# Kernel tuning notes

Measured on AMD Instinct MI355X. Metric: run time of the kernel, lower is better.

## Reference

```python
import jax, jax.numpy as jnp
import numpy as np

B_, J_, D_, E_, N_, K_ = 32, 1024, 192, 384, 16, 3


def _dwconv(x, w, b):
    # x: (B,J,E), w: (E,1,K) depthwise, b: (E,)
    xc = jnp.transpose(x, (0, 2, 1))  # (B,E,J)
    pad = w.shape[2] // 2
    y = jax.lax.conv_general_dilated(
        xc, w, window_strides=(1,), padding=[(pad, pad)],
        feature_group_count=w.shape[0], dimension_numbers=('NCH', 'OIH', 'NCH'))
    return jnp.transpose(y + b[None, :, None], (0, 2, 1))  # (B,J,E)


def _scan_dir(x, cw, cb, WB, bB, WC, bC, WD, bD, A, Wi, bi, Wr, br):
    # One directional selective-SSM pass. x: (B,J,E); A: (N,) negative diag.
    xc = _dwconv(x, cw, cb)                       # (B,J,E)
    Bt = xc @ WB + bB                             # (B,J,N)
    Ct = xc @ WC + bC                             # (B,J,N)
    Dt = jax.nn.softplus(xc @ WD + bD)            # Delta, (B,J,N)
    A_bar = jnp.exp(Dt * A)                       # ZOH discretization
    B_bar = (A_bar - 1.0) / (A + 1e-6) * Bt
    u = xc @ Wi + bi                              # in_to_state, (B,J,N)
    Bu = B_bar * u

    def step(h, ab_bu):
        ab, bu = ab_bu
        h = ab * h + bu
        return h, h

    h0 = jnp.zeros((x.shape[0], A.shape[0]), x.dtype)
    _, hs = jax.lax.scan(step, h0, (jnp.swapaxes(A_bar, 0, 1), jnp.swapaxes(Bu, 0, 1)))
    hs = jnp.swapaxes(hs, 0, 1)                   # (B,J,N)
    return (hs * Ct) @ Wr + br                    # readout, (B,J,E)


def setup_inputs() -> dict:
    key = jax.random.key(0)
    ks = iter(jax.random.split(key, 40))

    def nrm(shape, scale=0.02):
        return jax.random.normal(next(ks), shape, jnp.float32) * scale

    inp = {
        'tokens': jax.random.normal(next(ks), (B_, J_, D_), jnp.float32),
        'norm_g': jnp.ones((D_,), jnp.float32),
        'norm_b': jnp.zeros((D_,), jnp.float32),
        'Wx': nrm((D_, E_)), 'bx': jnp.zeros((E_,), jnp.float32),
        'Wz': nrm((D_, E_)), 'bz': jnp.zeros((E_,), jnp.float32),
        'convf_w': nrm((E_, 1, K_), 0.1), 'convf_b': jnp.zeros((E_,), jnp.float32),
        'convb_w': nrm((E_, 1, K_), 0.1), 'convb_b': jnp.zeros((E_,), jnp.float32),
        'WBf': nrm((E_, N_)), 'bBf': jnp.zeros((N_,), jnp.float32),
        'WCf': nrm((E_, N_)), 'bCf': jnp.zeros((N_,), jnp.float32),
        'WDf': nrm((E_, N_)), 'bDf': jnp.zeros((N_,), jnp.float32),
        'WBb': nrm((E_, N_)), 'bBb': jnp.zeros((N_,), jnp.float32),
        'WCb': nrm((E_, N_)), 'bCb': jnp.zeros((N_,), jnp.float32),
        'WDb': nrm((E_, N_)), 'bDb': jnp.zeros((N_,), jnp.float32),
        'A_log': nrm((N_,), 0.5),
        'Wi': nrm((E_, N_)), 'bi': jnp.zeros((N_,), jnp.float32),
        'Wr': nrm((N_, E_)), 'br': jnp.zeros((E_,), jnp.float32),
        'Wo': nrm((E_, D_)), 'bo': jnp.zeros((D_,), jnp.float32),
    }
    return inp


def reference(tokens, norm_g, norm_b, Wx, bx, Wz, bz, convf_w, convf_b,
              convb_w, convb_b, WBf, bBf, WCf, bCf, WDf, bDf, WBb, bBb,
              WCb, bCb, WDb, bDb, A_log, Wi, bi, Wr, br, Wo, bo):
    # LayerNorm (biased variance, eps=1e-5, like torch)
    mu = jnp.mean(tokens, axis=-1, keepdims=True)
    var = jnp.mean(jnp.square(tokens - mu), axis=-1, keepdims=True)
    t = (tokens - mu) / jnp.sqrt(var + 1e-5) * norm_g + norm_b

    x = t @ Wx + bx
    z = t @ Wz + bz
    gate = jax.nn.sigmoid(jax.nn.silu(z))

    # A computed under no_grad in torch -> stop_gradient here
    A = jax.lax.stop_gradient(-jax.nn.softplus(A_log))

    y_f = _scan_dir(x, convf_w, convf_b, WBf, bBf, WCf, bCf, WDf, bDf, A, Wi, bi, Wr, br)
    y_b = jnp.flip(_scan_dir(jnp.flip(x, 1), convb_w, convb_b, WBb, bBb, WCb, bCb,
                             WDb, bDb, A, Wi, bi, Wr, br), 1)
    y = (y_f + y_b) * gate
    return tokens + y @ Wo + bo
```

## Files before the change

kernel.cpp:

```cpp
#include <hip/hip_runtime.h>
#include <math.h>


typedef __attribute__((ext_vector_type(8))) short short8;
typedef __attribute__((ext_vector_type(4))) float f32x4;

__device__ __forceinline__ unsigned short f2bf(float f){
  union { float f; unsigned u; } v; v.f = f;
  unsigned r = v.u + 0x7FFFu + ((v.u >> 16) & 1u);
  return (unsigned short)(r >> 16);
}
__device__ __forceinline__ float bf2f(unsigned short s){
  union { unsigned u; float f; } v; v.u = ((unsigned)s) << 16;
  return v.f;
}
__device__ __forceinline__ float softplusf(float x){
  return (x > 20.f) ? x : log1pf(expf(x));
}
__device__ __forceinline__ float sigf_fast(float x){
  return __builtin_amdgcn_rcpf(1.f + __expf(-x));
}

__global__ __launch_bounds__(256) void prep_kernel(
    const float* __restrict__ Wx, const float* __restrict__ Wz,
    const float* __restrict__ WBf, const float* __restrict__ WCf,
    const float* __restrict__ WDf, const float* __restrict__ WBb,
    const float* __restrict__ WCb, const float* __restrict__ WDb,
    const float* __restrict__ Wi, const float* __restrict__ Wr,
    const float* __restrict__ Wo,
    const float* __restrict__ bBf, const float* __restrict__ bCf,
    const float* __restrict__ bDf, const float* __restrict__ bBb,
    const float* __restrict__ bCb, const float* __restrict__ bDb,
    const float* __restrict__ bi,
    unsigned short* __restrict__ Wxz_t, unsigned short* __restrict__ W4f_t,
    unsigned short* __restrict__ W4b_t, unsigned short* __restrict__ Wrt2,
    unsigned short* __restrict__ Wot, float* __restrict__ b4f,
    float* __restrict__ b4b)
{
  int idx = blockIdx.x * 256 + threadIdx.x;
  if (idx < 147456){ int n = idx / 192, k = idx % 192;
    Wxz_t[idx] = f2bf(n < 384 ? Wx[k*384 + n] : Wz[k*384 + n - 384]); return; }
  idx -= 147456;
  if (idx < 24576){ int n = idx / 384, k = idx % 384;
    const float* W = (n<16)?WBf:(n<32)?WCf:(n<48)?WDf:Wi;
    W4f_t[idx] = f2bf(W[k*16 + (n&15)]); return; }
  idx -= 24576;
  if (idx < 24576){ int n = idx / 384, k = idx % 384;
    const float* W = (n<16)?WBb:(n<32)?WCb:(n<48)?WDb:Wi;
    W4b_t[idx] = f2bf(W[k*16 + (n&15)]); return; }
  idx -= 24576;
  if (idx < 12288){ int n = idx / 32, k = idx % 32;
    Wrt2[idx] = f2bf(Wr[(k&15)*384 + n]); return; }
  idx -= 12288;
  if (idx < 73728){ int n = idx / 384, k = idx % 384;
    Wot[idx] = f2bf(Wo[k*192 + n]); return; }
  idx -= 73728;
  if (idx < 64){
    const float* bsel = (idx<16)?bBf:(idx<32)?bCf:(idx<48)?bDf:bi;
    b4f[idx] = bsel[idx & 15]; return; }
  idx -= 64;
  if (idx < 64){
    const float* bsel = (idx<16)?bBb:(idx<32)?bCb:(idx<48)?bDb:bi;
    b4b[idx] = bsel[idx & 15]; return; }
}

__global__ __launch_bounds__(512) void ln_xz_mfma(
    const float* __restrict__ tokens, const float* __restrict__ g,
    const float* __restrict__ nb, const unsigned short* __restrict__ Wxz_t,
    const float* __restrict__ bx, const float* __restrict__ bz,
    unsigned short* __restrict__ x_bf, unsigned short* __restrict__ gate_bf)
{
  __shared__ unsigned short t_lds[32 * 200];
  __shared__ unsigned short out_lds[16 * 784];
  const int t = threadIdx.x;
  const int row0 = blockIdx.x * 32;

  {
    const int r = t >> 4, l16 = t & 15;
    const float* tr = tokens + (long)(row0 + r) * 192;
    float v[12], s = 0.f, sq = 0.f;
#pragma unroll
    for (int i = 0; i < 12; i++){ float x = tr[l16 + 16*i]; v[i] = x; s += x; sq += x*x; }
#pragma unroll
    for (int m = 1; m < 16; m <<= 1){ s += __shfl_xor(s, m); sq += __shfl_xor(sq, m); }
    const float mu = s * (1.f/192.f);
    const float rstd = rsqrtf(sq * (1.f/192.f) - mu*mu + 1e-5f);
#pragma unroll
    for (int i = 0; i < 12; i++){
      const int d = l16 + 16*i;
      t_lds[r*200 + d] = f2bf((v[i] - mu)*rstd*g[d] + nb[d]);
    }
  }
  __syncthreads();

  const int lane = t & 63, w = t >> 6;
  const int c0 = w * 96;
  const int l15 = lane & 15, q = lane >> 4;
  f32x4 acc[2][6];
#pragma unroll
  for (int m = 0; m < 2; m++)
#pragma unroll
    for (int n = 0; n < 6; n++) acc[m][n] = (f32x4){0.f,0.f,0.f,0.f};

  const unsigned short* wb = Wxz_t + (long)(c0 + l15)*192 + q*8;
#pragma unroll
  for (int ks = 0; ks < 6; ks++){
    const int k0 = ks * 32;
    short8 a0 = *(const short8*)&t_lds[l15*200 + k0 + q*8];
    short8 a1 = *(const short8*)&t_lds[(16 + l15)*200 + k0 + q*8];
#pragma unroll
    for (int nf = 0; nf < 6; nf++){
      short8 bw = *(const short8*)&wb[nf*16*192 + k0];
      acc[0][nf] = __builtin_amdgcn_mfma_f32_16x16x32_bf16(a0, bw, acc[0][nf], 0, 0, 0);
      acc[1][nf] = __builtin_amdgcn_mfma_f32_16x16x32_bf16(a1, bw, acc[1][nf], 0, 0, 0);
    }
  }

#pragma unroll
  for (int m = 0; m < 2; m++){
#pragma unroll
    for (int nf = 0; nf < 6; nf++){
      const int c = c0 + nf*16 + l15;
      const int scol = c0 + ((nf + q) % 6)*16 + l15;
      if (c < 384){
        const float bv = bx[c];
#pragma unroll
        for (int r = 0; r < 4; r++)
          out_lds[(q*4 + r)*784 + scol] = f2bf(acc[m][nf][r] + bv);
      } else {
        const float bv = bz[c - 384];
#pragma unroll
        for (int r = 0; r < 4; r++){
          const float z = acc[m][nf][r] + bv;
          const float si = z * sigf_fast(z);
          out_lds[(q*4 + r)*784 + scol] = f2bf(sigf_fast(si));
        }
      }
    }
    __syncthreads();
    {
#pragma unroll
      for (int i = 0; i < 3; i++){
        const int item = i*512 + t;
        const int row  = item / 96;
        const int c_out = (item % 96) * 8;
        const int qq = (row >> 2) & 3;
        const int wsl = c_out / 96;
        const int nfl = (c_out % 96) / 16;
        const int scol = wsl*96 + ((nfl + qq) % 6)*16 + (c_out % 16);
        short8 v = *(const short8*)&out_lds[row*784 + scol];
        const long R = (long)row0 + m*16 + row;
        if (c_out < 384) *(short8*)&x_bf[R*384 + c_out] = v;
        else             *(short8*)&gate_bf[R*384 + (c_out - 384)] = v;
      }
    }
    __syncthreads();
  }
}

__global__ __launch_bounds__(256) void proj_mfma(
    const unsigned short* __restrict__ x_bf,
    const float* __restrict__ cwf, const float* __restrict__ cbf,
    const float* __restrict__ cwb, const float* __restrict__ cbb,
    const unsigned short* __restrict__ W4f, const unsigned short* __restrict__ W4b,
    const float* __restrict__ b4f, const float* __restrict__ b4b,
    const float* __restrict__ A_log,
    float* __restrict__ Af, float* __restrict__ Buf, float* __restrict__ Ctf,
    float* __restrict__ Ab, float* __restrict__ Bub, float* __restrict__ Ctb)
{
  __shared__ unsigned short xc[64 * 392];
  float* trans = (float*)xc;
  const int t = threadIdx.x;
  const int dir = blockIdx.x >> 9;
  const int bid = blockIdx.x & 511;
  const int b  = bid >> 4;
  const int j0 = (bid & 15) * 64;
  const float* cw = dir ? cwb : cwf;
  const float* cb = dir ? cbb : cbf;
  const unsigned short* W4 = dir ? W4b : W4f;
  const float* b4 = dir ? b4b : b4f;
  float* Aout = dir ? Ab  : Af;
  float* Bout = dir ? Bub : Buf;
  float* Cout = dir ? Ctb : Ctf;

  {
    const long xrow = (long)b * 1024 * 384;
#pragma unroll
    for (int i = 0; i < 12; i++){
      const int idx = i*256 + t;
      const int r = idx / 48;
      const int e0 = (idx - r*48) * 8;
      const int jp = j0 + r;
      short8 xm = (short8){0,0,0,0,0,0,0,0};
      short8 xp = (short8){0,0,0,0,0,0,0,0};
      if (jp >= 1){
        const int js = dir ? 1024 - jp : jp - 1;
        xm = *(const short8*)&x_bf[xrow + (long)js*384 + e0];
      }
      short8 x0;
      {
        const int js = dir ? 1023 - jp : jp;
        x0 = *(const short8*)&x_bf[xrow + (long)js*384 + e0];
      }
      if (jp <= 1022){
        const int js = dir ? 1022 - jp : jp + 1;
        xp = *(const short8*)&x_bf[xrow + (long)js*384 + e0];
      }
      float wv[24], cbv[8];
#pragma unroll
      for (int v = 0; v < 6; v++)
        *(float4*)&wv[v*4] = *(const float4*)&cw[e0*3 + v*4];
#pragma unroll
      for (int v = 0; v < 2; v++)
        *(float4*)&cbv[v*4] = *(const float4*)&cb[e0 + v*4];
      short8 o;
#pragma unroll
      for (int m = 0; m < 8; m++){
        const float acc = fmaf(wv[3*m],   bf2f((unsigned short)xm[m]),
                          fmaf(wv[3*m+1], bf2f((unsigned short)x0[m]),
                          fmaf(wv[3*m+2], bf2f((unsigned short)xp[m]), cbv[m])));
        o[m] = (short)f2bf(acc);
      }
      *(short8*)&xc[r*392 + e0] = o;
    }
  }
  __syncthreads();

  const int lane = t & 63, w = t >> 6;
  const int l15 = lane & 15, q = lane >> 4;
  f32x4 acc[4];
#pragma unroll
  for (int nf = 0; nf < 4; nf++) acc[nf] = (f32x4){0.f,0.f,0.f,0.f};
  const unsigned short* wb = W4 + (long)l15*384 + q*8;
#pragma unroll
  for (int ks = 0; ks < 12; ks++){
    const int k0 = ks * 32;
    short8 a = *(const short8*)&xc[(w*16 + l15)*392 + k0 + q*8];
#pragma unroll
    for (int nf = 0; nf < 4; nf++){
      short8 bw = *(const short8*)&wb[nf*16*384 + k0];
      acc[nf] = __builtin_amdgcn_mfma_f32_16x16x32_bf16(a, bw, acc[nf], 0, 0, 0);
    }
  }
  __syncthreads();

  {
    const int n = l15;
    const float Av = -softplusf(A_log[n]);
    const float bB = b4[n], bC = b4[16+n], bD = b4[32+n], bU = b4[48+n];
#pragma unroll
    for (int r = 0; r < 4; r++){
      const int row = w*16 + q*4 + r;
      const float Bt  = acc[0][r] + bB;
      const float Ctv = acc[1][r] + bC;
      const float dt  = softplusf(acc[2][r] + bD);
      const float u   = acc[3][r] + bU;
      const float ab  = expf(dt * Av);
      const float bu  = (ab - 1.f) / (Av + 1e-6f) * Bt * u;
      trans[(0*16 + n)*66 + row] = ab;
      trans[(1*16 + n)*66 + row] = bu;
      trans[(2*16 + n)*66 + row] = Ctv;
    }
  }
  __syncthreads();

  {
    const int j = t & 63, n4 = t >> 6;
#pragma unroll
    for (int i = 0; i < 4; i++){
      const int n = n4*4 + i;
      const int jp = j0 + j;
      const long base = ((long)b*16 + n) * 1024;
      Aout[base + jp] = trans[(0*16 + n)*66 + j];
      Bout[base + jp] = trans[(1*16 + n)*66 + j];
      Cout[base + (dir ? 1023 - jp : jp)] = trans[(2*16 + n)*66 + j];
    }
  }
}

__global__ __launch_bounds__(256) void scan2_kernel(
    const float* __restrict__ Af, const float* __restrict__ Buf, float* __restrict__ hsf,
    const float* __restrict__ Ab, const float* __restrict__ Bub, float* __restrict__ hsb)
{
  __shared__ float sA[256], sB[256];
  const int sel = blockIdx.x >> 9;
  const long base = (long)(blockIdx.x & 511) * 1024;
  const float* Abar = sel ? Ab  : Af;
  const float* Bu   = sel ? Bub : Buf;
  float* hs         = sel ? hsb : hsf;
  const int t = threadIdx.x;
  const float4 a4 = *reinterpret_cast<const float4*>(&Abar[base + t*4]);
  const float4 b4 = *reinterpret_cast<const float4*>(&Bu[base + t*4]);
  float A = a4.x, Bc = b4.x;
  Bc = fmaf(a4.y, Bc, b4.y); A *= a4.y;
  Bc = fmaf(a4.z, Bc, b4.z); A *= a4.z;
  Bc = fmaf(a4.w, Bc, b4.w); A *= a4.w;
  sA[t] = A; sB[t] = Bc;
  __syncthreads();
  for (int off = 1; off < 256; off <<= 1){
    const float cA = sA[t], cB = sB[t];
    float pA = 1.f, pB = 0.f;
    if (t >= off){ pA = sA[t - off]; pB = sB[t - off]; }
    __syncthreads();
    sA[t] = pA * cA;
    sB[t] = fmaf(cA, pB, cB);
    __syncthreads();
  }
  float h = (t > 0) ? sB[t - 1] : 0.f;
  float4 o;
  h = fmaf(a4.x, h, b4.x); o.x = h;
  h = fmaf(a4.y, h, b4.y); o.y = h;
  h = fmaf(a4.z, h, b4.z); o.z = h;
  h = fmaf(a4.w, h, b4.w); o.w = h;
  *reinterpret_cast<float4*>(&hs[base + t*4]) = o;
}

__global__ __launch_bounds__(256) void final_mfma(
    const float* __restrict__ tokens, const unsigned short* __restrict__ gate_bf,
    const float* __restrict__ hsf, const float* __restrict__ Ctf,
    const float* __restrict__ hsb, const float* __restrict__ Ctb,
    const unsigned short* __restrict__ Wrt2, const float* __restrict__ br,
    const unsigned short* __restrict__ Wot, const float* __restrict__ bo,
    float* __restrict__ out)
{
  __shared__ unsigned short s2[32 * 40];
  __shared__ unsigned short yg[32 * 392];
  const int t = threadIdx.x;
  const int b  = blockIdx.x >> 5;
  const int j0 = (blockIdx.x & 31) * 32;

  {
#pragma unroll
    for (int i = 0; i < 4; i++){
      const int idx = i*256 + t;
      const int j = idx & 31, kk = idx >> 5;
      float val;
      if (kk < 16){
        const long p = ((long)b*16 + kk)*1024 + j0 + j;
        val = hsf[p] * Ctf[p];
      } else {
        const long basen = ((long)b*16 + (kk - 16)) * 1024;
        val = hsb[basen + 1023 - (j0 + j)] * Ctb[basen + j0 + j];
      }
      s2[j*40 + kk] = f2bf(val);
    }
  }
  __syncthreads();

  const int lane = t & 63, w = t >> 6;
  const int l15 = lane & 15, q = lane >> 4;
  const int rt = w & 1;
  const int ng = w >> 1;

  {
    short8 a = *(const short8*)&s2[(rt*16 + l15)*40 + q*8];
    const unsigned short* wbp = Wrt2 + (long)l15*32 + q*8;
#pragma unroll
    for (int i = 0; i < 12; i++){
      const int nf = ng*12 + i;
      short8 bw = *(const short8*)&wbp[nf*16*32];
      f32x4 acc = (f32x4){0.f,0.f,0.f,0.f};
      acc = __builtin_amdgcn_mfma_f32_16x16x32_bf16(a, bw, acc, 0, 0, 0);
      const int c = nf*16 + l15;
      const float brv = 2.f * br[c];
#pragma unroll
      for (int r = 0; r < 4; r++)
        yg[(rt*16 + q*4 + r)*392 + c] = f2bf(acc[r] + brv);
    }
  }
  __syncthreads();

  {
#pragma unroll
    for (int i = 0; i < 6; i++){
      const int item = i*256 + t;
      const int row = item / 48;
      const int cb  = (item % 48) * 8;
      short8 y8 = *(const short8*)&yg[row*392 + cb];
      short8 g8 = *(const short8*)&gate_bf[((long)b*1024 + j0 + row)*384 + cb];
      short8 o;
#pragma unroll
      for (int m = 0; m < 8; m++)
        o[m] = (short)f2bf(bf2f((unsigned short)y8[m]) * bf2f((unsigned short)g8[m]));
      *(short8*)&yg[row*392 + cb] = o;
    }
  }
  __syncthreads();

  f32x4 acc[6];
  {
#pragma unroll
    for (int i = 0; i < 6; i++) acc[i] = (f32x4){0.f,0.f,0.f,0.f};
    const unsigned short* wbp = Wot + (long)l15*384 + q*8;
#pragma unroll
    for (int ks = 0; ks < 12; ks++){
      const int k0 = ks * 32;
      short8 a = *(const short8*)&yg[(rt*16 + l15)*392 + k0 + q*8];
#pragma unroll
      for (int i = 0; i < 6; i++){
        const int nf = ng*6 + i;
        short8 bw = *(const short8*)&wbp[(long)nf*16*384 + k0];
        acc[i] = __builtin_amdgcn_mfma_f32_16x16x32_bf16(a, bw, acc[i], 0, 0, 0);
      }
    }
  }
  __syncthreads();

  float* stg = (float*)yg;
  {
    const int gq = q ^ (q >> 1);
#pragma unroll
    for (int i = 0; i < 6; i++){
      const int nf = ng*6 + i;
      const int c = nf*16 + l15;
      const float bv = bo[c];
      const int scol = ((nf + gq) % 12)*16 + l15;
#pragma unroll
      for (int r = 0; r < 4; r++)
        stg[(rt*16 + q*4 + r)*196 + scol] = acc[i][r] + bv;
    }
  }
  __syncthreads();

  {
#pragma unroll
    for (int i = 0; i < 6; i++){
      const int item = i*256 + t;
      const int row = item / 48;
      const int c4  = (item % 48) * 4;
      const int qq = (row >> 2) & 3;
      const int gg = qq ^ (qq >> 1);
      const int nf = c4 / 16;
      const int scol = ((nf + gg) % 12)*16 + (c4 % 16);
      float4 v = *(const float4*)&stg[row*196 + scol];
      const long R = (long)b*1024 + j0 + row;
      const float4 tk = *(const float4*)&tokens[R*192 + c4];
      v.x += tk.x; v.y += tk.y; v.z += tk.z; v.w += tk.w;
      *(float4*)&out[R*192 + c4] = v;
    }
  }
}

extern "C" void kernel_launch(void* const* d_in, const int* in_sizes, int n_in,
                              void* d_out, int out_size, void* d_ws, size_t ws_size,
                              hipStream_t stream)
{
  const float* tokens  = (const float*)d_in[0];
  const float* norm_g  = (const float*)d_in[1];
  const float* norm_b  = (const float*)d_in[2];
  const float* Wx      = (const float*)d_in[3];
  const float* bx      = (const float*)d_in[4];
  const float* Wz      = (const float*)d_in[5];
  const float* bz      = (const float*)d_in[6];
  const float* convf_w = (const float*)d_in[7];
  const float* convf_b = (const float*)d_in[8];
  const float* convb_w = (const float*)d_in[9];
  const float* convb_b = (const float*)d_in[10];
  const float* WBf     = (const float*)d_in[11];
  const float* bBf     = (const float*)d_in[12];
  const float* WCf     = (const float*)d_in[13];
  const float* bCf     = (const float*)d_in[14];
  const float* WDf     = (const float*)d_in[15];
  const float* bDf     = (const float*)d_in[16];
  const float* WBb     = (const float*)d_in[17];
  const float* bBb     = (const float*)d_in[18];
  const float* WCb     = (const float*)d_in[19];
  const float* bCb     = (const float*)d_in[20];
  const float* WDb     = (const float*)d_in[21];
  const float* bDb     = (const float*)d_in[22];
  const float* A_log   = (const float*)d_in[23];
  const float* Wi      = (const float*)d_in[24];
  const float* bi      = (const float*)d_in[25];
  const float* Wr      = (const float*)d_in[26];
  const float* br      = (const float*)d_in[27];
  const float* Wo      = (const float*)d_in[28];
  const float* bo      = (const float*)d_in[29];

  char* ws = (char*)d_ws;
  unsigned short* x_bf    = (unsigned short*)(ws + 0);
  unsigned short* gate_bf = (unsigned short*)(ws + 25165824);
  unsigned short* Wxz_t   = (unsigned short*)(ws + 50331648);
  unsigned short* W4f_t   = (unsigned short*)(ws + 50626560);
  unsigned short* W4b_t   = (unsigned short*)(ws + 50675712);
  unsigned short* Wrt2    = (unsigned short*)(ws + 50724864);
  unsigned short* Wot     = (unsigned short*)(ws + 50749440);
  float* b4f = (float*)(ws + 50896896);
  float* b4b = (float*)(ws + 50897152);
  float* Af  = (float*)(ws + 50897408);
  float* Buf = (float*)(ws + 52994560);
  float* Ctf = (float*)(ws + 55091712);
  float* hsf = (float*)(ws + 57188864);
  float* Ab  = (float*)(ws + 59286016);
  float* Bub = (float*)(ws + 61383168);
  float* Ctb = (float*)(ws + 63480320);
  float* hsb = (float*)(ws + 65577472);

  prep_kernel<<<1105, 256, 0, stream>>>(Wx, Wz, WBf, WCf, WDf, WBb, WCb, WDb,
                                        Wi, Wr, Wo, bBf, bCf, bDf, bBb, bCb, bDb, bi,
                                        Wxz_t, W4f_t, W4b_t, Wrt2, Wot, b4f, b4b);
  ln_xz_mfma<<<1024, 512, 0, stream>>>(tokens, norm_g, norm_b, Wxz_t, bx, bz,
                                       x_bf, gate_bf);
  proj_mfma<<<1024, 256, 0, stream>>>(x_bf, convf_w, convf_b, convb_w, convb_b,
                                      W4f_t, W4b_t, b4f, b4b, A_log,
                                      Af, Buf, Ctf, Ab, Bub, Ctb);
  scan2_kernel<<<1024, 256, 0, stream>>>(Af, Buf, hsf, Ab, Bub, hsb);
  final_mfma<<<1024, 256, 0, stream>>>(tokens, gate_bf, hsf, Ctf, hsb, Ctb,
                                       Wrt2, br, Wot, bo, (float*)d_out);
}
```

Baseline: 150.0 us.

## Retile LayerNorm+xz GEMM to 64-row blocks split by x/z output half

The LayerNorm plus x/z projection kernel now gives each 256-thread block 64 rows and one output half (x or gate), instead of 512-thread blocks covering 32 rows and both halves. Each weight fragment load feeds four MFMA row tiles instead of two, raising weight reuse and removing the per-column branch between the x and gate epilogues. The output staging buffer now reuses the LayerNorm LDS tile, which reduces shared memory per block. In exchange, LayerNorm is recomputed for each row block by both column-half blocks, and each thread holds more accumulator registers.

```diff
diff --git a/kernel.cpp b/kernel.cpp
--- a/kernel.cpp
+++ b/kernel.cpp
@@ -64,31 +64,34 @@
     b4b[idx] = bsel[idx & 15]; return; }
 }
 
-__global__ __launch_bounds__(512) void ln_xz_mfma(
+__global__ __launch_bounds__(256, 4) void ln_xz_mfma(
     const float* __restrict__ tokens, const float* __restrict__ g,
     const float* __restrict__ nb, const unsigned short* __restrict__ Wxz_t,
     const float* __restrict__ bx, const float* __restrict__ bz,
     unsigned short* __restrict__ x_bf, unsigned short* __restrict__ gate_bf)
 {
-  __shared__ unsigned short t_lds[32 * 200];
-  __shared__ unsigned short out_lds[16 * 784];
+  __shared__ unsigned short t_lds[64 * 200];
   const int t = threadIdx.x;
-  const int row0 = blockIdx.x * 32;
-
-  {
-    const int r = t >> 4, l16 = t & 15;
-    const float* tr = tokens + (long)(row0 + r) * 192;
-    float v[12], s = 0.f, sq = 0.f;
-#pragma unroll
-    for (int i = 0; i < 12; i++){ float x = tr[l16 + 16*i]; v[i] = x; s += x; sq += x*x; }
-#pragma unroll
-    for (int m = 1; m < 16; m <<= 1){ s += __shfl_xor(s, m); sq += __shfl_xor(sq, m); }
-    const float mu = s * (1.f/192.f);
-    const float rstd = rsqrtf(sq * (1.f/192.f) - mu*mu + 1e-5f);
-#pragma unroll
-    for (int i = 0; i < 12; i++){
-      const int d = l16 + 16*i;
-      t_lds[r*200 + d] = f2bf((v[i] - mu)*rstd*g[d] + nb[d]);
+  const int ch = blockIdx.x & 1;
+  const int row0 = (blockIdx.x >> 1) * 64;
+
+  {
+#pragma unroll
+    for (int p = 0; p < 2; p++){
+      const int r = p*32 + (t >> 3), l8 = t & 7;
+      const float* tr = tokens + (long)(row0 + r) * 192;
+      float v[24], s = 0.f, sq = 0.f;
+#pragma unroll
+      for (int i = 0; i < 24; i++){ float x = tr[l8 + 8*i]; v[i] = x; s += x; sq += x*x; }
+#pragma unroll
+      for (int m = 1; m < 8; m <<= 1){ s += __shfl_xor(s, m); sq += __shfl_xor(sq, m); }
+      const float mu = s * (1.f/192.f);
+      const float rstd = rsqrtf(sq * (1.f/192.f) - mu*mu + 1e-5f);
+#pragma unroll
+      for (int i = 0; i < 24; i++){
+        const int d = l8 + 8*i;
+        t_lds[r*200 + d] = f2bf((v[i] - mu)*rstd*g[d] + nb[d]);
+      }
     }
   }
   __syncthreads();
@@ -96,62 +99,73 @@
   const int lane = t & 63, w = t >> 6;
   const int c0 = w * 96;
   const int l15 = lane & 15, q = lane >> 4;
-  f32x4 acc[2][6];
-#pragma unroll
-  for (int m = 0; m < 2; m++)
+  f32x4 acc[4][6];
+#pragma unroll
+  for (int m = 0; m < 4; m++)
 #pragma unroll
     for (int n = 0; n < 6; n++) acc[m][n] = (f32x4){0.f,0.f,0.f,0.f};
 
-  const unsigned short* wb = Wxz_t + (long)(c0 + l15)*192 + q*8;
+  const unsigned short* wb = Wxz_t + (long)(ch*384 + c0 + l15)*192 + q*8;
 #pragma unroll
   for (int ks = 0; ks < 6; ks++){
     const int k0 = ks * 32;
-    short8 a0 = *(const short8*)&t_lds[l15*200 + k0 + q*8];
+    short8 a0 = *(const short8*)&t_lds[(     l15)*200 + k0 + q*8];
     short8 a1 = *(const short8*)&t_lds[(16 + l15)*200 + k0 + q*8];
+    short8 a2 = *(const short8*)&t_lds[(32 + l15)*200 + k0 + q*8];
+    short8 a3 = *(const short8*)&t_lds[(48 + l15)*200 + k0 + q*8];
 #pragma unroll
     for (int nf = 0; nf < 6; nf++){
       short8 bw = *(const short8*)&wb[nf*16*192 + k0];
       acc[0][nf] = __builtin_amdgcn_mfma_f32_16x16x32_bf16(a0, bw, acc[0][nf], 0, 0, 0);
       acc[1][nf] = __builtin_amdgcn_mfma_f32_16x16x32_bf16(a1, bw, acc[1][nf], 0, 0, 0);
-    }
-  }
-
-#pragma unroll
-  for (int m = 0; m < 2; m++){
-#pragma unroll
-    for (int nf = 0; nf < 6; nf++){
-      const int c = c0 + nf*16 + l15;
-      const int scol = c0 + ((nf + q) % 6)*16 + l15;
-      if (c < 384){
-        const float bv = bx[c];
-#pragma unroll
-        for (int r = 0; r < 4; r++)
-          out_lds[(q*4 + r)*784 + scol] = f2bf(acc[m][nf][r] + bv);
-      } else {
-        const float bv = bz[c - 384];
-#pragma unroll
-        for (int r = 0; r < 4; r++){
-          const float z = acc[m][nf][r] + bv;
-          const float si = z * sigf_fast(z);
-          out_lds[(q*4 + r)*784 + scol] = f2bf(sigf_fast(si));
+      acc[2][nf] = __builtin_amdgcn_mfma_f32_16x16x32_bf16(a2, bw, acc[2][nf], 0, 0, 0);
+      acc[3][nf] = __builtin_amdgcn_mfma_f32_16x16x32_bf16(a3, bw, acc[3][nf], 0, 0, 0);
+    }
+  }
+  __syncthreads();
+
+  const float* bias = ch ? bz : bx;
+  unsigned short* outp = ch ? gate_bf : x_bf;
+  unsigned short* stage = t_lds;
+
+#pragma unroll
+  for (int pp = 0; pp < 2; pp++){
+#pragma unroll
+    for (int mm = 0; mm < 2; mm++){
+      const int m = pp*2 + mm;
+#pragma unroll
+      for (int nf = 0; nf < 6; nf++){
+        const int lc = c0 + nf*16 + l15;
+        const int scol = c0 + ((nf + q) % 6)*16 + l15;
+        const float bv = bias[lc];
+        if (ch == 0){
+#pragma unroll
+          for (int r = 0; r < 4; r++)
+            stage[(mm*16 + q*4 + r)*392 + scol] = f2bf(acc[m][nf][r] + bv);
+        } else {
+#pragma unroll
+          for (int r = 0; r < 4; r++){
+            const float z = acc[m][nf][r] + bv;
+            const float si = z * sigf_fast(z);
+            stage[(mm*16 + q*4 + r)*392 + scol] = f2bf(sigf_fast(si));
+          }
         }
       }
     }
     __syncthreads();
     {
 #pragma unroll
-      for (int i = 0; i < 3; i++){
-        const int item = i*512 + t;
-        const int row  = item / 96;
-        const int c_out = (item % 96) * 8;
+      for (int i = 0; i < 6; i++){
+        const int item = i*256 + t;
+        const int row  = item / 48;
+        const int c_out = (item % 48) * 8;
         const int qq = (row >> 2) & 3;
         const int wsl = c_out / 96;
         const int nfl = (c_out % 96) / 16;
         const int scol = wsl*96 + ((nfl + qq) % 6)*16 + (c_out % 16);
-        short8 v = *(const short8*)&out_lds[row*784 + scol];
-        const long R = (long)row0 + m*16 + row;
-        if (c_out < 384) *(short8*)&x_bf[R*384 + c_out] = v;
-        else             *(short8*)&gate_bf[R*384 + (c_out - 384)] = v;
+        short8 v = *(const short8*)&stage[row*392 + scol];
+        const long R = (long)row0 + pp*32 + row;
+        *(short8*)&outp[R*384 + c_out] = v;
       }
     }
     __syncthreads();
@@ -498,7 +512,7 @@
   prep_kernel<<<1105, 256, 0, stream>>>(Wx, Wz, WBf, WCf, WDf, WBb, WCb, WDb,
                                         Wi, Wr, Wo, bBf, bCf, bDf, bBb, bCb, bDb, bi,
                                         Wxz_t, W4f_t, W4b_t, Wrt2, Wot, b4f, b4b);
-  ln_xz_mfma<<<1024, 512, 0, stream>>>(tokens, norm_g, norm_b, Wxz_t, bx, bz,
+  ln_xz_mfma<<<1024, 256, 0, stream>>>(tokens, norm_g, norm_b, Wxz_t, bx, bz,
                                        x_bf, gate_bf);
   proj_mfma<<<1024, 256, 0, stream>>>(x_bf, convf_w, convf_b, convb_w, convb_b,
                                       W4f_t, W4b_t, b4f, b4b, A_log,
```

After: 170.1 us. 1.13x slower.
